# Kernel optimization log

Hardware: AMD Instinct MI355X
Metric: run time of the kernel (lower is better)

The kernel has to match this reference:

```python
import jax, jax.numpy as jnp
import numpy as np

# Segmented tensor-product configuration (matches init_kwargs)
NUM_SEG = 32   # segments per operand
MUL = 128      # multiplicity ('u' axis) of operand0 / output segments
D = 3          # irrep dimension (2l+1 with l=1) for i, j, k axes
NUM_PATHS = 64
BATCH = 2048


def setup_inputs() -> dict:
    key = jax.random.key(0)
    k0, k1, k2, k3, k4, k5 = jax.random.split(key, 6)
    x0 = jax.random.normal(k0, (BATCH, NUM_SEG * MUL * D), dtype=jnp.float32)
    x1 = jax.random.normal(k1, (BATCH, NUM_SEG * D), dtype=jnp.float32)
    coeff = jax.random.normal(k2, (NUM_PATHS, D, D, D), dtype=jnp.float32)
    idx0 = jax.random.randint(k3, (NUM_PATHS,), 0, NUM_SEG, dtype=jnp.int32)
    idx1 = jax.random.randint(k4, (NUM_PATHS,), 0, NUM_SEG, dtype=jnp.int32)
    idx2 = jax.random.randint(k5, (NUM_PATHS,), 0, NUM_SEG, dtype=jnp.int32)
    return {"x0": x0, "x1": x1, "coeff": coeff,
            "idx0": idx0, "idx1": idx1, "idx2": idx2}


def reference(x0, x1, coeff, idx0, idx1, idx2):
    # Segmented CG tensor product:
    #   out[seg2][u,k] += sum_{paths p with idx2[p]==seg2}
    #       sum_ij x0[idx0[p]][u,i] * x1[idx1[p]][j] * coeff[p][i,j,k]
    B = x0.shape[0]
    x0s = x0.reshape(B, NUM_SEG, MUL, D)   # 'ui' segments
    x1s = x1.reshape(B, NUM_SEG, D)        # 'j' segments
    # gather input segments per path
    x0p = x0s[:, idx0]                     # (B, P, MUL, D)
    x1p = x1s[:, idx1]                     # (B, P, D)
    # per-path contraction with path coefficients, path axis first for scatter
    contrib = jnp.einsum('bpui,bpj,pijk->pbuk', x0p, x1p, coeff)
    # scatter-add contributions into output segments
    out_seg = jax.ops.segment_sum(contrib, idx2, num_segments=NUM_SEG)  # (S, B, MUL, D)
    out = jnp.transpose(out_seg, (1, 0, 2, 3)).reshape(B, NUM_SEG * MUL * D)
    return out
```

## Files before the change

kernel.cpp:

```cpp
#include <hip/hip_runtime.h>

#define NUM_SEG 32
#define MUL 128
#define D 3
#define NUM_PATHS 64
#define ROW (NUM_SEG * MUL * D)

__global__ __launch_bounds__(256) void ftp_kernel(
    const float* __restrict__ x0, const float* __restrict__ x1,
    const float* __restrict__ coeff, const int* __restrict__ idx0,
    const int* __restrict__ idx1, const int* __restrict__ idx2,
    float* __restrict__ out)
{
    const int b   = blockIdx.x;
    const int tid = threadIdx.x;

    __shared__ float s_m[NUM_PATHS][D * D];
    __shared__ int   s_seg0[NUM_PATHS];
    __shared__ unsigned char s_plist[NUM_SEG][NUM_PATHS];
    __shared__ int   s_cnt[NUM_SEG];

    if (tid < NUM_SEG) s_cnt[tid] = 0;
    __syncthreads();

    if (tid < NUM_PATHS) {
        const int p  = tid;
        const int i1 = idx1[p];
        s_seg0[p]    = idx0[p];
        const int s2 = idx2[p];
        const int pos = atomicAdd(&s_cnt[s2], 1);
        s_plist[s2][pos] = (unsigned char)p;

        const float* x1row = x1 + (size_t)b * (NUM_SEG * D) + i1 * D;
        const float xj0 = x1row[0], xj1 = x1row[1], xj2 = x1row[2];
        const float* cf = coeff + p * 27;
        #pragma unroll
        for (int i = 0; i < D; ++i) {
            #pragma unroll
            for (int k = 0; k < D; ++k) {
                s_m[p][i * 3 + k] = xj0 * cf[i * 9 + 0 + k]
                                  + xj1 * cf[i * 9 + 3 + k]
                                  + xj2 * cf[i * 9 + 6 + k];
            }
        }
    }
    __syncthreads();

    const int u  = tid & (MUL - 1);
    const int sg = tid >> 7;
    const float* __restrict__ x0row = x0 + (size_t)b * ROW + u * D;
    float* __restrict__ outrow = out + (size_t)b * ROW + u * D;

    for (int s = sg; s < NUM_SEG; s += 2) {
        float acc0 = 0.f, acc1 = 0.f, acc2 = 0.f;
        const int n = s_cnt[s];
        for (int t = 0; t < n; ++t) {
            const int p = s_plist[s][t];
            const float* xs = x0row + s_seg0[p] * (MUL * D);
            const float a0 = xs[0], a1 = xs[1], a2 = xs[2];
            const float* m = s_m[p];
            acc0 += a0 * m[0] + a1 * m[3] + a2 * m[6];
            acc1 += a0 * m[1] + a1 * m[4] + a2 * m[7];
            acc2 += a0 * m[2] + a1 * m[5] + a2 * m[8];
        }
        float* o = outrow + s * (MUL * D);
        __builtin_nontemporal_store(acc0, o + 0);
        __builtin_nontemporal_store(acc1, o + 1);
        __builtin_nontemporal_store(acc2, o + 2);
    }
}

extern "C" void kernel_launch(void* const* d_in, const int* in_sizes, int n_in,
                              void* d_out, int out_size, void* d_ws, size_t ws_size,
                              hipStream_t stream) {
    const float* x0    = (const float*)d_in[0];
    const float* x1    = (const float*)d_in[1];
    const float* coeff = (const float*)d_in[2];
    const int*   idx0  = (const int*)d_in[3];
    const int*   idx1  = (const int*)d_in[4];
    const int*   idx2  = (const int*)d_in[5];
    float* out = (float*)d_out;

    const int B = in_sizes[0] / ROW;
    ftp_kernel<<<B, 256, 0, stream>>>(x0, x1, coeff, idx0, idx1, idx2, out);
}
```

Before: 204.5 us.

## Precompute sorted path schedule in setup kernel and process paths as a flat stream

A one-block setup kernel sorts the paths by output segment, packs seg0, path id and a flush flag into a schedule in workspace, and lists the empty output segments. The main kernel handles four batch rows per block. Each thread covers two u entries (six floats) with v2f loads and walks all 64 paths in one fully unrolled loop, writing its accumulators out whenever a segment ends. This removes the per-block shared-memory atomics, the per-segment loop and its divergence, and adds an extra kernel launch, a dependence on the workspace, plain stores in place of nontemporal ones, and a separate zero-fill pass for empty segments.

```diff
diff --git a/kernel.cpp b/kernel.cpp
--- a/kernel.cpp
+++ b/kernel.cpp
@@ -5,68 +5,114 @@
 #define D 3
 #define NUM_PATHS 64
 #define ROW (NUM_SEG * MUL * D)
+#define SEGF (MUL * D)
+#define RPB 4
 
-__global__ __launch_bounds__(256) void ftp_kernel(
+typedef float v2f __attribute__((ext_vector_type(2)));
+typedef float v4f __attribute__((ext_vector_type(4)));
+
+__global__ __launch_bounds__(64) void setup_kernel(
+    const int* __restrict__ idx0, const int* __restrict__ idx2,
+    int* __restrict__ ws)
+{
+    __shared__ int s2[NUM_PATHS];
+    __shared__ int ord[NUM_PATHS];
+    __shared__ int has[NUM_SEG];
+    __shared__ int ecnt;
+    const int t = threadIdx.x;
+    if (t < NUM_SEG) has[t] = 0;
+    if (t == 0) ecnt = 0;
+    s2[t] = idx2[t];
+    __syncthreads();
+    const int key = s2[t] * 64 + t;
+    int rank = 0;
+    for (int p = 0; p < NUM_PATHS; ++p) rank += ((s2[p] * 64 + p) < key);
+    ord[rank] = t;
+    has[s2[t]] = 1;
+    __syncthreads();
+    const int p = ord[t];
+    const int fl = (t == NUM_PATHS - 1 || s2[ord[t + 1]] != s2[p]) ? s2[p] : 255;
+    ws[t] = (idx0[p] & 255) | ((p & 255) << 8) | (fl << 16);
+    if (t < NUM_SEG && !has[t]) {
+        const int slot = atomicAdd(&ecnt, 1);
+        ws[65 + slot] = t;
+    }
+    __syncthreads();
+    if (t == 0) ws[64] = ecnt;
+}
+
+__global__ __launch_bounds__(256) void ftp_main(
     const float* __restrict__ x0, const float* __restrict__ x1,
-    const float* __restrict__ coeff, const int* __restrict__ idx0,
-    const int* __restrict__ idx1, const int* __restrict__ idx2,
-    float* __restrict__ out)
+    const float* __restrict__ coeff, const int* __restrict__ idx1,
+    const int* __restrict__ ws, float* __restrict__ out)
 {
-    const int b   = blockIdx.x;
+    __shared__ float s_m[RPB][NUM_PATHS][12];
+    __shared__ int s_sched[NUM_PATHS];
+    __shared__ int s_emp[33];
+
     const int tid = threadIdx.x;
+    const int b0 = blockIdx.x * RPB;
 
-    __shared__ float s_m[NUM_PATHS][D * D];
-    __shared__ int   s_seg0[NUM_PATHS];
-    __shared__ unsigned char s_plist[NUM_SEG][NUM_PATHS];
-    __shared__ int   s_cnt[NUM_SEG];
+    if (tid < 64) s_sched[tid] = ws[tid];
+    else if (tid < 97) s_emp[tid - 64] = ws[tid];
 
-    if (tid < NUM_SEG) s_cnt[tid] = 0;
-    __syncthreads();
-
-    if (tid < NUM_PATHS) {
-        const int p  = tid;
+    {
+        const int p = tid & 63, r = tid >> 6;
+        const int b = b0 + r;
         const int i1 = idx1[p];
-        s_seg0[p]    = idx0[p];
-        const int s2 = idx2[p];
-        const int pos = atomicAdd(&s_cnt[s2], 1);
-        s_plist[s2][pos] = (unsigned char)p;
-
-        const float* x1row = x1 + (size_t)b * (NUM_SEG * D) + i1 * D;
-        const float xj0 = x1row[0], xj1 = x1row[1], xj2 = x1row[2];
+        const float* xr = x1 + (size_t)b * (NUM_SEG * D) + i1 * D;
+        const float j0 = xr[0], j1 = xr[1], j2 = xr[2];
         const float* cf = coeff + p * 27;
         #pragma unroll
-        for (int i = 0; i < D; ++i) {
+        for (int i = 0; i < D; ++i)
             #pragma unroll
-            for (int k = 0; k < D; ++k) {
-                s_m[p][i * 3 + k] = xj0 * cf[i * 9 + 0 + k]
-                                  + xj1 * cf[i * 9 + 3 + k]
-                                  + xj2 * cf[i * 9 + 6 + k];
-            }
-        }
+            for (int k = 0; k < D; ++k)
+                s_m[r][p][i * 3 + k] = j0 * cf[i * 9 + k]
+                                     + j1 * cf[i * 9 + 3 + k]
+                                     + j2 * cf[i * 9 + 6 + k];
     }
     __syncthreads();
 
-    const int u  = tid & (MUL - 1);
-    const int sg = tid >> 7;
-    const float* __restrict__ x0row = x0 + (size_t)b * ROW + u * D;
-    float* __restrict__ outrow = out + (size_t)b * ROW + u * D;
+    const int q = tid & 63;
+    const int r = tid >> 6;
+    const int b = b0 + r;
+    const float* __restrict__ xb = x0 + (size_t)b * ROW + q * 6;
+    float* __restrict__ ob = out + (size_t)b * ROW + q * 6;
 
-    for (int s = sg; s < NUM_SEG; s += 2) {
-        float acc0 = 0.f, acc1 = 0.f, acc2 = 0.f;
-        const int n = s_cnt[s];
-        for (int t = 0; t < n; ++t) {
-            const int p = s_plist[s][t];
-            const float* xs = x0row + s_seg0[p] * (MUL * D);
-            const float a0 = xs[0], a1 = xs[1], a2 = xs[2];
-            const float* m = s_m[p];
-            acc0 += a0 * m[0] + a1 * m[3] + a2 * m[6];
-            acc1 += a0 * m[1] + a1 * m[4] + a2 * m[7];
-            acc2 += a0 * m[2] + a1 * m[5] + a2 * m[8];
+    float a00 = 0, a01 = 0, a02 = 0, a10 = 0, a11 = 0, a12 = 0;
+    #pragma unroll
+    for (int t = 0; t < NUM_PATHS; ++t) {
+        const int e = s_sched[t];
+        const int seg0 = e & 255;
+        const int p = (e >> 8) & 255;
+        const int fl = e >> 16;
+        const float* xs = xb + seg0 * SEGF;
+        const v2f L0 = *(const v2f*)(xs + 0);
+        const v2f L1 = *(const v2f*)(xs + 2);
+        const v2f L2 = *(const v2f*)(xs + 4);
+        const float* m = s_m[r][p];
+        a00 += L0.x * m[0] + L0.y * m[3] + L1.x * m[6];
+        a01 += L0.x * m[1] + L0.y * m[4] + L1.x * m[7];
+        a02 += L0.x * m[2] + L0.y * m[5] + L1.x * m[8];
+        a10 += L1.y * m[0] + L2.x * m[3] + L2.y * m[6];
+        a11 += L1.y * m[1] + L2.x * m[4] + L2.y * m[7];
+        a12 += L1.y * m[2] + L2.x * m[5] + L2.y * m[8];
+        if (fl != 255) {
+            float* o = ob + fl * SEGF;
+            v2f O0 = {a00, a01}, O1 = {a02, a10}, O2 = {a11, a12};
+            *(v2f*)(o + 0) = O0;
+            *(v2f*)(o + 2) = O1;
+            *(v2f*)(o + 4) = O2;
+            a00 = a01 = a02 = a10 = a11 = a12 = 0.f;
         }
-        float* o = outrow + s * (MUL * D);
-        __builtin_nontemporal_store(acc0, o + 0);
-        __builtin_nontemporal_store(acc1, o + 1);
-        __builtin_nontemporal_store(acc2, o + 2);
+    }
+    const int ne = s_emp[0];
+    for (int i = 0; i < ne; ++i) {
+        float* o = ob + s_emp[1 + i] * SEGF;
+        v2f Z = {0.f, 0.f};
+        *(v2f*)(o + 0) = Z;
+        *(v2f*)(o + 2) = Z;
+        *(v2f*)(o + 4) = Z;
     }
 }
 
@@ -80,7 +126,9 @@
     const int*   idx1  = (const int*)d_in[4];
     const int*   idx2  = (const int*)d_in[5];
     float* out = (float*)d_out;
+    int*   ws  = (int*)d_ws;
 
     const int B = in_sizes[0] / ROW;
-    ftp_kernel<<<B, 256, 0, stream>>>(x0, x1, coeff, idx0, idx1, idx2, out);
+    setup_kernel<<<1, 64, 0, stream>>>(idx0, idx2, ws);
+    ftp_main<<<B / RPB, 256, 0, stream>>>(x0, x1, coeff, idx1, ws, out);
 }
```

New measurement: 201.4 us. About the same (-1.5%).

## Stage half-row of x0 in LDS and split each batch row across two blocks

Applied to the files above, without the earlier changes.

Each block now handles half of the MUL axis for one batch row. It loads that half of x0 into shared memory with coalesced float4 loads and then does the gathered per-path reads from LDS instead of global memory. Each thread computes two u values per segment and writes float2 vector stores, where the old code used nontemporal scalar stores. The aim is to replace repeated scattered global gathers of x0 with one coalesced load, at the cost of 24KB LDS per block and the per-block setup work being done twice.

```diff
diff --git a/kernel.cpp b/kernel.cpp
--- a/kernel.cpp
+++ b/kernel.cpp
@@ -5,6 +5,12 @@
 #define D 3
 #define NUM_PATHS 64
 #define ROW (NUM_SEG * MUL * D)
+#define SEGF (MUL * D)
+#define HALF_F4 1536
+#define SEG_HF 192
+
+typedef float v2f __attribute__((ext_vector_type(2)));
+typedef float v4f __attribute__((ext_vector_type(4)));
 
 __global__ __launch_bounds__(256) void ftp_kernel(
     const float* __restrict__ x0, const float* __restrict__ x1,
@@ -12,61 +18,77 @@
     const int* __restrict__ idx1, const int* __restrict__ idx2,
     float* __restrict__ out)
 {
-    const int b   = blockIdx.x;
+    const int bid = blockIdx.x;
+    const int b   = bid >> 1;
+    const int h   = bid & 1;
     const int tid = threadIdx.x;
 
-    __shared__ float s_m[NUM_PATHS][D * D];
-    __shared__ int   s_seg0[NUM_PATHS];
-    __shared__ unsigned char s_plist[NUM_SEG][NUM_PATHS];
+    __shared__ v4f   s_x0[HALF_F4];
+    __shared__ float s_m[NUM_PATHS][9];
+    __shared__ unsigned short s_pe[NUM_SEG][NUM_PATHS];
     __shared__ int   s_cnt[NUM_SEG];
 
     if (tid < NUM_SEG) s_cnt[tid] = 0;
     __syncthreads();
 
+    const v4f* __restrict__ src = (const v4f*)(x0 + (size_t)b * ROW);
+    #pragma unroll
+    for (int j = 0; j < 6; ++j) {
+        const int f     = j * 256 + tid;
+        const int seg   = f / 48;
+        const int inner = f - seg * 48;
+        s_x0[f] = src[seg * 96 + h * 48 + inner];
+    }
+
     if (tid < NUM_PATHS) {
         const int p  = tid;
+        const int s0 = idx0[p];
         const int i1 = idx1[p];
-        s_seg0[p]    = idx0[p];
         const int s2 = idx2[p];
         const int pos = atomicAdd(&s_cnt[s2], 1);
-        s_plist[s2][pos] = (unsigned char)p;
+        s_pe[s2][pos] = (unsigned short)(s0 | (p << 8));
 
-        const float* x1row = x1 + (size_t)b * (NUM_SEG * D) + i1 * D;
-        const float xj0 = x1row[0], xj1 = x1row[1], xj2 = x1row[2];
+        const float* xr = x1 + (size_t)b * (NUM_SEG * D) + i1 * D;
+        const float j0 = xr[0], j1 = xr[1], j2 = xr[2];
         const float* cf = coeff + p * 27;
         #pragma unroll
-        for (int i = 0; i < D; ++i) {
+        for (int i = 0; i < D; ++i)
             #pragma unroll
-            for (int k = 0; k < D; ++k) {
-                s_m[p][i * 3 + k] = xj0 * cf[i * 9 + 0 + k]
-                                  + xj1 * cf[i * 9 + 3 + k]
-                                  + xj2 * cf[i * 9 + 6 + k];
-            }
-        }
+            for (int k = 0; k < D; ++k)
+                s_m[p][i * 3 + k] = j0 * cf[i * 9 + k]
+                                  + j1 * cf[i * 9 + 3 + k]
+                                  + j2 * cf[i * 9 + 6 + k];
     }
     __syncthreads();
 
-    const int u  = tid & (MUL - 1);
-    const int sg = tid >> 7;
-    const float* __restrict__ x0row = x0 + (size_t)b * ROW + u * D;
-    float* __restrict__ outrow = out + (size_t)b * ROW + u * D;
+    const int q  = tid & 31;
+    const int ss = tid >> 5;
+    float* __restrict__ ob = out + (size_t)b * ROW + h * SEG_HF + q * 6;
+    const float* __restrict__ sx = (const float*)s_x0;
 
-    for (int s = sg; s < NUM_SEG; s += 2) {
-        float acc0 = 0.f, acc1 = 0.f, acc2 = 0.f;
+    #pragma unroll
+    for (int si = 0; si < 4; ++si) {
+        const int s = ss + si * 8;
+        float a00 = 0, a01 = 0, a02 = 0, a10 = 0, a11 = 0, a12 = 0;
         const int n = s_cnt[s];
         for (int t = 0; t < n; ++t) {
-            const int p = s_plist[s][t];
-            const float* xs = x0row + s_seg0[p] * (MUL * D);
-            const float a0 = xs[0], a1 = xs[1], a2 = xs[2];
-            const float* m = s_m[p];
-            acc0 += a0 * m[0] + a1 * m[3] + a2 * m[6];
-            acc1 += a0 * m[1] + a1 * m[4] + a2 * m[7];
-            acc2 += a0 * m[2] + a1 * m[5] + a2 * m[8];
+            const int e = s_pe[s][t];
+            const float* xs = sx + (e & 255) * SEG_HF + q * 6;
+            const float u00 = xs[0], u01 = xs[1], u02 = xs[2];
+            const float u10 = xs[3], u11 = xs[4], u12 = xs[5];
+            const float* m = s_m[e >> 8];
+            a00 += u00 * m[0] + u01 * m[3] + u02 * m[6];
+            a01 += u00 * m[1] + u01 * m[4] + u02 * m[7];
+            a02 += u00 * m[2] + u01 * m[5] + u02 * m[8];
+            a10 += u10 * m[0] + u11 * m[3] + u12 * m[6];
+            a11 += u10 * m[1] + u11 * m[4] + u12 * m[7];
+            a12 += u10 * m[2] + u11 * m[5] + u12 * m[8];
         }
-        float* o = outrow + s * (MUL * D);
-        __builtin_nontemporal_store(acc0, o + 0);
-        __builtin_nontemporal_store(acc1, o + 1);
-        __builtin_nontemporal_store(acc2, o + 2);
+        float* o = ob + s * SEGF;
+        v2f O0 = {a00, a01}, O1 = {a02, a10}, O2 = {a11, a12};
+        *(v2f*)(o + 0) = O0;
+        *(v2f*)(o + 2) = O1;
+        *(v2f*)(o + 4) = O2;
     }
 }
 
@@ -82,5 +104,5 @@
     float* out = (float*)d_out;
 
     const int B = in_sizes[0] / ROW;
-    ftp_kernel<<<B, 256, 0, stream>>>(x0, x1, coeff, idx0, idx1, idx2, out);
+    ftp_kernel<<<B * 2, 256, 0, stream>>>(x0, x1, coeff, idx0, idx1, idx2, out);
 }
```

After: 190.3 us. 1.07x faster.
